# Kernel tuning notes

Hardware: AMD Instinct MI355X
Metric: run time of the kernel (lower is better)

## Reference

```python
import jax, jax.numpy as jnp
import numpy as np

DILATIONS = [1, 2, 4, 8, 16, 32, 64, 128, 256, 512] * 2
WD = 128   # residual/gate channels
SD = 512   # skip channels
VOCAB = 256
FIELD = int(np.sum(DILATIONS)) + 2  # receptive field = 2048


def setup_inputs() -> dict:
    key = jax.random.key(0)
    ks = jax.random.split(key, 10)
    B, T = 4, 16384
    L = len(DILATIONS)
    y = jax.random.randint(ks[0], (B, T), 0, VOCAB)
    embed = jax.random.normal(ks[1], (VOCAB, WD), dtype=jnp.float32) * 0.1
    # dilated causal conv: kernel_size=2, wd -> 2*wd (gate stacking)
    Wd = jax.random.normal(ks[2], (L, 2 * WD, WD, 2), dtype=jnp.float32) * 0.05
    bd = jnp.zeros((L, 2 * WD), dtype=jnp.float32)
    # skip 1x1 conv: wd -> sd
    Ws = jax.random.normal(ks[3], (L, SD, WD, 1), dtype=jnp.float32) * 0.05
    bs = jnp.zeros((L, SD), dtype=jnp.float32)
    # residual 1x1 conv: wd -> wd
    Wr = jax.random.normal(ks[4], (L, WD, WD, 1), dtype=jnp.float32) * 0.05
    br = jnp.zeros((L, WD), dtype=jnp.float32)
    # post convs (bias=False)
    W1 = jax.random.normal(ks[5], (SD, SD, 1), dtype=jnp.float32) * 0.05
    W2 = jax.random.normal(ks[6], (VOCAB, SD, 1), dtype=jnp.float32) * 0.05
    return {"y": y, "embed": embed, "Wd": Wd, "bd": bd, "Ws": Ws,
            "bs": bs, "Wr": Wr, "br": br, "W1": W1, "W2": W2}


def reference(y, embed, Wd, bd, Ws, bs, Wr, br, W1, W2):
    # embedding -> [B, C, T]
    x = jnp.transpose(embed[y], (0, 2, 1))
    finalout = x.shape[2] - (FIELD - 1)
    skip = None
    for i, d in enumerate(DILATIONS):
        # dilated valid conv with kernel size 2 == two shifted 1x1 matmuls
        in_act = (jnp.einsum('oc,bct->bot', Wd[i, :, :, 0], x[:, :, :-d]) +
                  jnp.einsum('oc,bct->bot', Wd[i, :, :, 1], x[:, :, d:]) +
                  bd[i][None, :, None])                       # [B, 2*WD, T-d]
        acts = jnp.tanh(in_act[:, :WD]) * jax.nn.sigmoid(in_act[:, WD:])
        res = jnp.einsum('oc,bct->bot', Wr[i, :, :, 0], acts) + br[i][None, :, None]
        sk = (jnp.einsum('oc,bct->bot', Ws[i, :, :, 0], acts[:, :, -finalout:]) +
              bs[i][None, :, None])                            # [B, SD, finalout]
        skip = sk if skip is None else skip + sk
        x = res + x[:, :, d:]
    out = jax.nn.relu(skip)
    out = jax.nn.relu(jnp.einsum('oc,bct->bot', W1[:, :, 0], out))
    out = jnp.einsum('oc,bct->bot', W2[:, :, 0], out)          # [B, 256, finalout]
    return out
```

## Files before the change

### kernel.cpp

```cpp
#include <hip/hip_runtime.h>
#include <cstddef>

#define B_    4
#define T_    16384
#define FOUT_ 14337
#define FOUTP 14464
#define NL_   20
#define XSTR  ((size_t)T_*128)
#define ABSTR ((size_t)FOUTP*128)
#define ALSTR ((size_t)B_*FOUTP*128)
#define SBSTR ((size_t)FOUTP*512)

typedef float    f32x16 __attribute__((ext_vector_type(16)));
typedef _Float16 f16x8  __attribute__((ext_vector_type(8)));

__device__ _Float16 g_xh0[(size_t)B_*T_*128];
__device__ _Float16 g_xh1[(size_t)B_*T_*128];
__device__ _Float16 g_WdF0[(size_t)NL_*256*128];
__device__ _Float16 g_WdF1[(size_t)NL_*256*128];
__device__ _Float16 g_WrF [(size_t)NL_*128*128];
__device__ _Float16 g_WsF [(size_t)512*2560];
__device__ _Float16 g_W1F [(size_t)512*512];
__device__ _Float16 g_W2F [(size_t)256*512];
__device__ float    g_bssum[512];
__device__ _Float16 g_acts[(size_t)NL_*B_*FOUTP*128];
__device__ _Float16 g_skipF[(size_t)B_*FOUTP*512];
__device__ _Float16 g_h1F [(size_t)B_*FOUTP*512];

__device__ __forceinline__ float sigm_(float x){ return 1.0f/(1.0f+__expf(-x)); }
__device__ __forceinline__ float tanh_(float x){ return 1.0f - 2.0f/(__expf(2.0f*x)+1.0f); }
__device__ __forceinline__ f32x16 MFMA32(f16x8 a, f16x8 b, f32x16 c){
  return __builtin_amdgcn_mfma_f32_32x32x16_f16(a, b, c, 0, 0, 0);
}

__global__ void cvt_wd(const float* __restrict__ Wd){
  int i = blockIdx.x*256 + threadIdx.x;
  if (i >= NL_*256*16) return;
  int row = i >> 4, koct = i & 15;
  const float* s = Wd + ((size_t)row*128 + koct*8)*2;
  int lane = (koct&1)*32 + (row&31);
  size_t addr = (size_t)((row>>5)*8 + (koct>>1))*512 + lane*8;
  union { _Float16 h[8]; uint4 v; } u0, u1;
#pragma unroll
  for (int j=0;j<8;j++){ u0.h[j]=(_Float16)s[2*j]; u1.h[j]=(_Float16)s[2*j+1]; }
  *(uint4*)((void*)(g_WdF0 + addr)) = u0.v;
  *(uint4*)((void*)(g_WdF1 + addr)) = u1.v;
}
__global__ void cvt_rm(const float* __restrict__ src, int which, int M, int K){
  int i = blockIdx.x*256 + threadIdx.x;
  if (i >= M*(K>>3)) return;
  int row = i / (K>>3), koct = i % (K>>3);
  const float* s = src + (size_t)row*K + koct*8;
  int lane = (koct&1)*32 + (row&31);
  size_t addr = ((size_t)(row>>5)*(K>>4) + (koct>>1))*512 + lane*8;
  union { _Float16 h[8]; uint4 v; } u;
#pragma unroll
  for (int j=0;j<8;j++) u.h[j]=(_Float16)s[j];
  _Float16* dst = (which==0)?g_WrF:(which==1)?g_W1F:g_W2F;
  *(uint4*)((void*)(dst + addr)) = u.v;
}
__global__ void cvt_ws(const float* __restrict__ Ws){
  int i = blockIdx.x*256 + threadIdx.x;
  if (i >= NL_*512*16) return;
  int l = i >> 13, o = (i>>4)&511, coct = i&15;
  const float* s = Ws + ((size_t)(l*512+o))*128 + coct*8;
  int lane = (coct&1)*32 + (o&31);
  size_t addr = ((size_t)(o>>5)*160 + (size_t)(l*8 + (coct>>1)))*512 + lane*8;
  union { _Float16 h[8]; uint4 v; } u;
#pragma unroll
  for (int j=0;j<8;j++) u.h[j]=(_Float16)s[j];
  *(uint4*)((void*)(g_WsF + addr)) = u.v;
}
__global__ void bssum_k(const float* __restrict__ bs){
  int o = threadIdx.x;
  float s = 0.f;
  for (int l=0;l<NL_;l++) s += bs[l*512 + o];
  g_bssum[o] = s;
}

__global__ void embed_kernel(const int* __restrict__ y, const float* __restrict__ embed){
  int gid = blockIdx.x*256 + threadIdx.x;
  int bt = gid >> 4, c8 = gid & 15;
  if (bt < B_*T_){
    int idx = y[bt];
    const float* e = embed + (size_t)idx*128 + c8*8;
    union { _Float16 h[8]; uint4 v; } u;
#pragma unroll
    for (int j=0;j<8;j++) u.h[j]=(_Float16)e[j];
    *(uint4*)((void*)(g_xh0 + (size_t)bt*128 + c8*8)) = u.v;
  }
}

__global__ __launch_bounds__(256,3) void layer16(
    int swap, int l, int d, int Tout, int ss,
    const float* __restrict__ bd_l, const float* __restrict__ br_l)
{
  const _Float16* __restrict__ xin  = swap ? g_xh1 : g_xh0;
  _Float16* __restrict__       xout = swap ? g_xh0 : g_xh1;

  __shared__ _Float16 X0s[16*520];
  __shared__ _Float16 X1s[16*520];
  __shared__ _Float16 ACs[16*520];

  const int tid = threadIdx.x;
  const int w   = tid >> 6;
  const int lane= tid & 63;
  const int ln2 = lane & 31;
  const int h   = lane >> 5;
  const int b   = blockIdx.y;
  const int t0  = blockIdx.x*64;
  const int ntv = min(64, Tout - t0);
  const int limit = Tout + d - 1;
  const _Float16* __restrict__ xb = xin + (size_t)b*XSTR;

#pragma unroll
  for (int it=0; it<4; it++){
    int t = (tid>>4) + it*16, c16 = tid&15;
    int s0 = t0 + t;     if (s0 > limit) s0 = limit;
    int s1 = t0 + t + d; if (s1 > limit) s1 = limit;
    *(uint4*)((void*)&X0s[c16*520 + t*8]) = *(const uint4*)((const void*)(xb + (size_t)s0*128 + c16*8));
    *(uint4*)((void*)&X1s[c16*520 + t*8]) = *(const uint4*)((const void*)(xb + (size_t)s1*128 + c16*8));
  }
  __syncthreads();

  f32x16 aB[2][2];
#pragma unroll
  for (int mi=0;mi<2;mi++)
#pragma unroll
    for (int nt=0;nt<2;nt++)
#pragma unroll
      for (int r=0;r<16;r++) aB[mi][nt][r] = 0.f;

#pragma unroll
  for (int tap=0; tap<2; tap++){
    const _Float16* __restrict__ Xs = tap ? X1s : X0s;
    const _Float16* __restrict__ Wt = (tap ? g_WdF1 : g_WdF0) + (size_t)l*32768;
    const _Float16* aT = Wt + (size_t)w*4096 + lane*8;
    const _Float16* aS = Wt + (size_t)(4+w)*4096 + lane*8;
#pragma unroll
    for (int ks=0; ks<8; ks++){
      f16x8 bfr[2];
#pragma unroll
      for (int nt=0; nt<2; nt++)
        bfr[nt] = *(const f16x8*)((const void*)&Xs[(ks*2+h)*520 + (nt*32+ln2)*8]);
      f16x8 fT = *(const f16x8*)((const void*)(aT + ks*512));
      f16x8 fS = *(const f16x8*)((const void*)(aS + ks*512));
#pragma unroll
      for (int nt=0; nt<2; nt++){
        aB[0][nt] = MFMA32(fT, bfr[nt], aB[0][nt]);
        aB[1][nt] = MFMA32(fS, bfr[nt], aB[1][nt]);
      }
    }
  }

#pragma unroll
  for (int nt=0; nt<2; nt++)
#pragma unroll
    for (int rq=0; rq<4; rq++){
      int c0 = w*32 + rq*8 + 4*h;
      union { _Float16 hh[4]; ushort4 v; } pk;
#pragma unroll
      for (int rr=0; rr<4; rr++){
        float it_ = aB[0][nt][rq*4+rr] + bd_l[c0+rr];
        float is_ = aB[1][nt][rq*4+rr] + bd_l[128+c0+rr];
        pk.hh[rr] = (_Float16)(tanh_(it_)*sigm_(is_));
      }
      *(ushort4*)((void*)&ACs[(w*4+rq)*520 + (nt*32+ln2)*8 + 4*h]) = pk.v;
    }
  __syncthreads();

  f32x16 aC[2];
#pragma unroll
  for (int nt=0;nt<2;nt++)
#pragma unroll
    for (int r=0;r<16;r++) aC[nt][r] = 0.f;
  {
    const _Float16* aW = g_WrF + (size_t)l*16384 + (size_t)w*4096 + lane*8;
#pragma unroll
    for (int ks=0; ks<8; ks++){
      f16x8 bfr[2];
#pragma unroll
      for (int nt=0; nt<2; nt++)
        bfr[nt] = *(const f16x8*)((const void*)&ACs[(ks*2+h)*520 + (nt*32+ln2)*8]);
      f16x8 fW = *(const f16x8*)((const void*)(aW + ks*512));
#pragma unroll
      for (int nt=0; nt<2; nt++)
        aC[nt] = MFMA32(fW, bfr[nt], aC[nt]);
    }
  }

#pragma unroll
  for (int nt=0; nt<2; nt++){
    int t = nt*32 + ln2;
    if (t < ntv){
      size_t xrow = (size_t)b*XSTR + (size_t)(t0+t)*128;
#pragma unroll
      for (int rq=0; rq<4; rq++){
        int c0 = w*32 + rq*8 + 4*h;
        union { ushort4 v; _Float16 hh[4]; } xr;
        xr.v = *(const ushort4*)((const void*)&X1s[(w*4+rq)*520 + t*8 + 4*h]);
        union { _Float16 hh[4]; ushort4 v; } ov;
#pragma unroll
        for (int rr=0; rr<4; rr++)
          ov.hh[rr] = (_Float16)(aC[nt][rq*4+rr] + br_l[c0+rr] + (float)xr.hh[rr]);
        *(ushort4*)((void*)(xout + xrow + c0)) = ov.v;
      }
    }
  }

  _Float16* __restrict__ actsB = g_acts + (size_t)l*ALSTR + (size_t)b*ABSTR;
#pragma unroll
  for (int it=0; it<4; it++){
    int t = (tid>>4) + it*16, c16 = tid&15;
    int ts = t0 + t - ss;
    if (t < ntv && ts >= 0 && ts < FOUT_){
      size_t addr = (size_t)(ts>>5)*4096 + (size_t)(c16>>1)*512 + ((c16&1)*32 + (ts&31))*8;
      *(uint4*)((void*)(actsB + addr)) = *(const uint4*)((const void*)&ACs[c16*520 + t*8]);
    }
  }
}

template<int MODE>
__global__ __launch_bounds__(512,2) void gemm_stream(float* __restrict__ outF){
  constexpr int NSTEP = (MODE==0)?160:32;
  constexpr int MFR   = (MODE==2)?1:2;
  const _Float16* __restrict__ A    = (MODE==0)?g_WsF:(MODE==1)?g_W1F:g_W2F;
  const _Float16* __restrict__ Bsrc = (MODE==0)?g_acts:(MODE==1)?g_skipF:g_h1F;

  const int tid = threadIdx.x;
  const int w   = tid >> 6;
  const int lane= tid & 63;
  const int ln2 = lane & 31;
  const int h   = lane >> 5;
  const int b   = blockIdx.y;
  const int ts0 = blockIdx.x*128;

  const _Float16* Bb[4];
#pragma unroll
  for (int nt=0;nt<4;nt++){
    size_t tile = blockIdx.x*4 + nt;
    Bb[nt] = (MODE==0) ? (Bsrc + (size_t)b*ABSTR + tile*4096 + lane*8)
                       : (Bsrc + (size_t)b*SBSTR + tile*16384 + lane*8);
  }
  const _Float16* Ab[2];
#pragma unroll
  for (int mi=0;mi<MFR;mi++)
    Ab[mi] = A + (size_t)(w*MFR+mi)*((size_t)NSTEP*512) + lane*8;

  f32x16 acc[2][4];
#pragma unroll
  for (int mi=0;mi<MFR;mi++)
#pragma unroll
    for (int nt=0;nt<4;nt++)
#pragma unroll
      for (int r=0;r<16;r++) acc[mi][nt][r] = 0.f;

#define BADDR(nt,s) ((MODE==0) ? (Bb[nt] + (size_t)((s)>>3)*ALSTR + (size_t)((s)&7)*512) \
                               : (Bb[nt] + (size_t)(s)*512))

  f16x8 Ae[2], Ao[2], Be[4], Bo[4];
#pragma unroll
  for (int mi=0;mi<MFR;mi++){
    Ae[mi] = *(const f16x8*)((const void*)(Ab[mi]));
    Ao[mi] = *(const f16x8*)((const void*)(Ab[mi] + 512));
  }
#pragma unroll
  for (int nt=0;nt<4;nt++){
    Be[nt] = *(const f16x8*)((const void*)BADDR(nt,0));
    Bo[nt] = *(const f16x8*)((const void*)BADDR(nt,1));
  }

  for (int s=0; s<NSTEP; s+=2){
#pragma unroll
    for (int mi=0;mi<MFR;mi++)
#pragma unroll
      for (int nt=0;nt<4;nt++)
        acc[mi][nt] = MFMA32(Ae[mi], Be[nt], acc[mi][nt]);
    if (s+2 < NSTEP){
#pragma unroll
      for (int mi=0;mi<MFR;mi++) Ae[mi] = *(const f16x8*)((const void*)(Ab[mi] + (size_t)(s+2)*512));
#pragma unroll
      for (int nt=0;nt<4;nt++)   Be[nt] = *(const f16x8*)((const void*)BADDR(nt,s+2));
    }
#pragma unroll
    for (int mi=0;mi<MFR;mi++)
#pragma unroll
      for (int nt=0;nt<4;nt++)
        acc[mi][nt] = MFMA32(Ao[mi], Bo[nt], acc[mi][nt]);
    if (s+3 < NSTEP){
#pragma unroll
      for (int mi=0;mi<MFR;mi++) Ao[mi] = *(const f16x8*)((const void*)(Ab[mi] + (size_t)(s+3)*512));
#pragma unroll
      for (int nt=0;nt<4;nt++)   Bo[nt] = *(const f16x8*)((const void*)BADDR(nt,s+3));
    }
  }
#undef BADDR

  if (MODE != 2){
    _Float16* __restrict__ dstb = ((MODE==0)?g_skipF:g_h1F) + (size_t)b*SBSTR;
#pragma unroll
    for (int mi=0; mi<MFR; mi++){
      int mtile = w*MFR+mi;
#pragma unroll
      for (int nt=0; nt<4; nt++){
        int ts = ts0 + nt*32 + ln2;
        if (ts >= FOUT_) continue;
#pragma unroll
        for (int rq=0; rq<4; rq++){
          int m0 = mtile*32 + rq*8 + 4*h;
          union { _Float16 hh[4]; ushort4 v; } pk;
#pragma unroll
          for (int rr=0; rr<4; rr++){
            float vv = acc[mi][nt][rq*4+rr];
            if (MODE==0) vv += g_bssum[m0+rr];
            pk.hh[rr] = (_Float16)fmaxf(vv, 0.f);
          }
          size_t addr = (size_t)(ts>>5)*16384 + (size_t)(mtile*2 + (rq>>1))*512
                      + ((rq&1)*32 + (ts&31))*8 + 4*h;
          *(ushort4*)((void*)(dstb + addr)) = pk.v;
        }
      }
    }
  } else {
#pragma unroll
    for (int nt=0; nt<4; nt++){
      int ts = ts0 + nt*32 + ln2;
      if (ts >= FOUT_) continue;
#pragma unroll
      for (int rq=0; rq<4; rq++){
        int m0 = w*32 + rq*8 + 4*h;
#pragma unroll
        for (int rr=0; rr<4; rr++)
          outF[((size_t)(b*256 + m0 + rr))*FOUT_ + ts] = acc[0][nt][rq*4+rr];
      }
    }
  }
}

extern "C" void kernel_launch(void* const* d_in, const int* in_sizes, int n_in,
                              void* d_out, int out_size, void* d_ws, size_t ws_size,
                              hipStream_t stream) {
  const int*   y     = (const int*)  d_in[0];
  const float* embed = (const float*)d_in[1];
  const float* Wd    = (const float*)d_in[2];
  const float* bd    = (const float*)d_in[3];
  const float* Ws    = (const float*)d_in[4];
  const float* bs    = (const float*)d_in[5];
  const float* Wr    = (const float*)d_in[6];
  const float* br    = (const float*)d_in[7];
  const float* W1    = (const float*)d_in[8];
  const float* W2    = (const float*)d_in[9];
  float* out = (float*)d_out;
  (void)d_ws; (void)ws_size;

  cvt_wd<<<dim3(320), dim3(256), 0, stream>>>(Wd);
  cvt_rm<<<dim3(160), dim3(256), 0, stream>>>(Wr, 0, NL_*128, 128);
  cvt_rm<<<dim3(128), dim3(256), 0, stream>>>(W1, 1, 512, 512);
  cvt_rm<<<dim3( 64), dim3(256), 0, stream>>>(W2, 2, 256, 512);
  cvt_ws<<<dim3(640), dim3(256), 0, stream>>>(Ws);
  bssum_k<<<dim3(1), dim3(512), 0, stream>>>(bs);

  embed_kernel<<<dim3((B_*T_*16)/256), dim3(256), 0, stream>>>(y, embed);

  static const int DIL[NL_] = {1,2,4,8,16,32,64,128,256,512,
                               1,2,4,8,16,32,64,128,256,512};
  int swap = 0;
  int Tin = T_;
  for (int i=0;i<NL_;i++){
    int d = DIL[i];
    int Tout = Tin - d;
    dim3 grid((Tout+63)/64, B_);
    layer16<<<grid, dim3(256), 0, stream>>>(
        swap, i, d, Tout, Tout - FOUT_, bd + (size_t)i*256, br + (size_t)i*128);
    swap ^= 1;
    Tin = Tout;
  }

  dim3 gg(FOUTP/128, B_);
  gemm_stream<0><<<gg, dim3(512), 0, stream>>>(nullptr);
  gemm_stream<1><<<gg, dim3(512), 0, stream>>>(nullptr);
  gemm_stream<2><<<gg, dim3(512), 0, stream>>>(out);
}
```

Before: 1.028 ms.

## Stage shared B tiles in LDS via double-buffered global_load_lds in gemm_stream

After: 972.5 us. 1.06x faster.

```diff
diff --git a/kernel.cpp b/kernel.cpp
--- a/kernel.cpp
+++ b/kernel.cpp
@@ -33,6 +33,12 @@
   return __builtin_amdgcn_mfma_f32_32x32x16_f16(a, b, c, 0, 0, 0);
 }
 
+typedef const __attribute__((address_space(1))) _Float16 gash;
+typedef __attribute__((address_space(3))) _Float16 lash;
+__device__ __forceinline__ void gld_lds16(const _Float16* g, _Float16* l){
+  __builtin_amdgcn_global_load_lds((gash*)g, (lash*)l, 16, 0, 0);
+}
+
 __global__ void cvt_wd(const float* __restrict__ Wd){
   int i = blockIdx.x*256 + threadIdx.x;
   if (i >= NL_*256*16) return;
@@ -223,9 +229,12 @@
 template<int MODE>
 __global__ __launch_bounds__(512,2) void gemm_stream(float* __restrict__ outF){
   constexpr int NSTEP = (MODE==0)?160:32;
+  constexpr int NCH   = NSTEP/8;
   constexpr int MFR   = (MODE==2)?1:2;
   const _Float16* __restrict__ A    = (MODE==0)?g_WsF:(MODE==1)?g_W1F:g_W2F;
   const _Float16* __restrict__ Bsrc = (MODE==0)?g_acts:(MODE==1)?g_skipF:g_h1F;
+
+  __shared__ __align__(16) _Float16 Bs[2][16384];
 
   const int tid = threadIdx.x;
   const int w   = tid >> 6;
@@ -235,19 +244,21 @@
   const int b   = blockIdx.y;
   const int ts0 = blockIdx.x*128;
 
-  const _Float16* Bb[4];
+  const _Float16* Gb[4];
 #pragma unroll
   for (int nt=0;nt<4;nt++){
     size_t tile = blockIdx.x*4 + nt;
-    Bb[nt] = (MODE==0) ? (Bsrc + (size_t)b*ABSTR + tile*4096 + lane*8)
+    Gb[nt] = (MODE==0) ? (Bsrc + (size_t)b*ABSTR + tile*4096  + lane*8)
                        : (Bsrc + (size_t)b*SBSTR + tile*16384 + lane*8);
   }
-  const _Float16* Ab[2];
+  const size_t cstr = (MODE==0) ? (size_t)ALSTR : (size_t)4096;
+
+  const _Float16* Ab[MFR];
 #pragma unroll
   for (int mi=0;mi<MFR;mi++)
     Ab[mi] = A + (size_t)(w*MFR+mi)*((size_t)NSTEP*512) + lane*8;
 
-  f32x16 acc[2][4];
+  f32x16 acc[MFR][4];
 #pragma unroll
   for (int mi=0;mi<MFR;mi++)
 #pragma unroll
@@ -255,46 +266,43 @@
 #pragma unroll
       for (int r=0;r<16;r++) acc[mi][nt][r] = 0.f;
 
-#define BADDR(nt,s) ((MODE==0) ? (Bb[nt] + (size_t)((s)>>3)*ALSTR + (size_t)((s)&7)*512) \
-                               : (Bb[nt] + (size_t)(s)*512))
-
-  f16x8 Ae[2], Ao[2], Be[4], Bo[4];
-#pragma unroll
-  for (int mi=0;mi<MFR;mi++){
-    Ae[mi] = *(const f16x8*)((const void*)(Ab[mi]));
-    Ao[mi] = *(const f16x8*)((const void*)(Ab[mi] + 512));
-  }
-#pragma unroll
-  for (int nt=0;nt<4;nt++){
-    Be[nt] = *(const f16x8*)((const void*)BADDR(nt,0));
-    Bo[nt] = *(const f16x8*)((const void*)BADDR(nt,1));
-  }
-
-  for (int s=0; s<NSTEP; s+=2){
-#pragma unroll
-    for (int mi=0;mi<MFR;mi++)
+  auto STAGE = [&](int buf, int c){
+#pragma unroll
+    for (int nt=0;nt<4;nt++){
+      const _Float16* g = Gb[nt] + (size_t)c*cstr + (size_t)w*512;
+      gld_lds16(g, &Bs[buf][((size_t)(w*4+nt))*512]);
+    }
+  };
+
+  auto COMPUTE = [&](int buf, int c){
+#pragma unroll
+    for (int ks=0; ks<8; ks++){
+      f16x8 bfr[4];
 #pragma unroll
       for (int nt=0;nt<4;nt++)
-        acc[mi][nt] = MFMA32(Ae[mi], Be[nt], acc[mi][nt]);
-    if (s+2 < NSTEP){
-#pragma unroll
-      for (int mi=0;mi<MFR;mi++) Ae[mi] = *(const f16x8*)((const void*)(Ab[mi] + (size_t)(s+2)*512));
-#pragma unroll
-      for (int nt=0;nt<4;nt++)   Be[nt] = *(const f16x8*)((const void*)BADDR(nt,s+2));
-    }
-#pragma unroll
-    for (int mi=0;mi<MFR;mi++)
-#pragma unroll
-      for (int nt=0;nt<4;nt++)
-        acc[mi][nt] = MFMA32(Ao[mi], Bo[nt], acc[mi][nt]);
-    if (s+3 < NSTEP){
-#pragma unroll
-      for (int mi=0;mi<MFR;mi++) Ao[mi] = *(const f16x8*)((const void*)(Ab[mi] + (size_t)(s+3)*512));
-#pragma unroll
-      for (int nt=0;nt<4;nt++)   Bo[nt] = *(const f16x8*)((const void*)BADDR(nt,s+3));
-    }
-  }
-#undef BADDR
+        bfr[nt] = *(const f16x8*)((const void*)&Bs[buf][(size_t)(ks*4+nt)*512 + lane*8]);
+      f16x8 af[MFR];
+#pragma unroll
+      for (int mi=0;mi<MFR;mi++)
+        af[mi] = *(const f16x8*)((const void*)(Ab[mi] + ((size_t)c*8 + ks)*512));
+#pragma unroll
+      for (int mi=0;mi<MFR;mi++)
+#pragma unroll
+        for (int nt=0;nt<4;nt++)
+          acc[mi][nt] = MFMA32(af[mi], bfr[nt], acc[mi][nt]);
+    }
+  };
+
+  STAGE(0, 0);
+  asm volatile("s_waitcnt vmcnt(0)" ::: "memory");
+  __syncthreads();
+  int cur = 0;
+  for (int c=0; c<NCH; ++c){
+    if (c+1 < NCH) STAGE(cur^1, c+1);
+    COMPUTE(cur, c);
+    __syncthreads();
+    cur ^= 1;
+  }
 
   if (MODE != 2){
     _Float16* __restrict__ dstb = ((MODE==0)?g_skipF:g_h1F) + (size_t)b*SBSTR;
```
